# Kernel optimization log

Hardware: AMD Instinct MI355X
Metric: run time of the kernel (lower is better)

Reference implementation:

```python
import jax, jax.numpy as jnp
import numpy as np

EPS = 1e-16


def setup_inputs() -> dict:
    key = jax.random.key(0)
    k1, k2 = jax.random.split(key)
    p = jax.random.normal(k1, (2, 32, 2048, 4), dtype=jnp.float32)
    q = jax.random.normal(k2, (32, 2048, 4), dtype=jnp.float32)
    return {"p": p, "q": q}


def reference(p, q):
    # im=False path: take the real part of the complex generated momenta
    p_real = p[0]                      # (B, N, 4)
    # loss_norm_choice='p3', take_sqrt=True: use 3-momenta (drop energy)
    p3 = p_real[..., 1:]               # (B, N, 3)
    q3 = q[..., 1:]                    # (B, M, 3)
    # Pairwise Euclidean distance (cdist) via the expanded quadratic form to
    # avoid materializing the (B, N, M, 3) difference tensor.
    x2 = jnp.sum(p3 * p3, axis=-1)     # (B, N)
    y2 = jnp.sum(q3 * q3, axis=-1)     # (B, M)
    xy = jnp.einsum('bnd,bmd->bnm', p3, q3)  # (B, N, M)
    dist_sq = x2[..., :, None] + y2[..., None, :] - 2.0 * xy
    dist = jnp.sqrt(jnp.maximum(dist_sq, 0.0) + EPS)  # (B, N, M)
    # Bidirectional nearest-neighbor min-reduction
    min_pq = jnp.min(dist, axis=-1)    # (B, N)
    min_qp = jnp.min(dist, axis=-2)    # (B, M)
    chamfer_loss = jnp.sum((min_pq + min_qp) * 0.5)
    return chamfer_loss
```

## Files before the change

kernel.cpp:

```cpp
#include <hip/hip_runtime.h>
#include <math.h>


#define NPTS   2048
#define NBATCH 32
#define NTOT   (2 * NBATCH * NPTS)
#define EPSF   1e-16f
#define BIGF   3.4e38f

__device__ __forceinline__ float min3f(float a, float b, float c) {
    return fminf(fminf(a, b), c);
}

__global__ __launch_bounds__(256) void chamfer_tile_kernel(
    const float* __restrict__ P, const float* __restrict__ Q,
    unsigned int* __restrict__ ws)
{
    __shared__ float4 sp[256];
    __shared__ float4 sq[256];
    __shared__ float  scol[4][256];

    const int tid = threadIdx.x;
    const int tx  = tid & 15;
    const int ty  = tid >> 4;
    const int bi  = blockIdx.x;
    const int bj  = blockIdx.y;
    const int b   = blockIdx.z;

    {
        float4 pv = ((const float4*)P)[(size_t)b * NPTS + bi * 256 + tid];
        sp[tid] = make_float4(pv.y, pv.z, pv.w,
                              pv.y*pv.y + pv.z*pv.z + pv.w*pv.w);
        float4 qv = ((const float4*)Q)[(size_t)b * NPTS + bj * 256 + tid];
        sq[tid] = make_float4(-2.f*qv.y, -2.f*qv.z, -2.f*qv.w,
                              qv.y*qv.y + qv.z*qv.z + qv.w*qv.w);
    }
    __syncthreads();

    float px[16], py[16], pz[16], x2[16];
    #pragma unroll
    for (int k = 0; k < 16; ++k) {
        float4 v = sp[ty + 16 * k];
        px[k] = v.x; py[k] = v.y; pz[k] = v.z; x2[k] = v.w;
    }

    float rowacc[16], colacc[16];
    #pragma unroll
    for (int k = 0; k < 16; ++k) { rowacc[k] = BIGF; colacc[k] = BIGF; }

    for (int jp = 0; jp < 8; ++jp) {
        float4 q0 = sq[tx + 32 * jp];
        float4 q1 = sq[tx + 32 * jp + 16];
        float c0 = BIGF, c1 = BIGF;
        #pragma unroll
        for (int k = 0; k < 16; k += 2) {
            float t00 = fmaf(px[k],   q0.x, fmaf(py[k],   q0.y, pz[k]   * q0.z));
            float t01 = fmaf(px[k],   q1.x, fmaf(py[k],   q1.y, pz[k]   * q1.z));
            float t10 = fmaf(px[k+1], q0.x, fmaf(py[k+1], q0.y, pz[k+1] * q0.z));
            float t11 = fmaf(px[k+1], q1.x, fmaf(py[k+1], q1.y, pz[k+1] * q1.z));
            rowacc[k]   = min3f(rowacc[k],   t00 + q0.w, t01 + q1.w);
            rowacc[k+1] = min3f(rowacc[k+1], t10 + q0.w, t11 + q1.w);
            c0 = min3f(c0, t00 + x2[k], t10 + x2[k+1]);
            c1 = min3f(c1, t01 + x2[k], t11 + x2[k+1]);
        }
        colacc[2*jp]     = c0;
        colacc[2*jp + 1] = c1;
    }

    #pragma unroll
    for (int k = 0; k < 16; ++k) {
        float v = rowacc[k];
        v = fminf(v, __shfl_xor(v, 1));
        v = fminf(v, __shfl_xor(v, 2));
        v = fminf(v, __shfl_xor(v, 4));
        v = fminf(v, __shfl_xor(v, 8));
        rowacc[k] = v;
    }
    if (tx == 0) {
        #pragma unroll
        for (int k = 0; k < 16; ++k) {
            float d2 = fmaxf(x2[k] + rowacc[k], 0.f);
            atomicMin(&ws[b * NPTS + bi * 256 + (ty + 16 * k)],
                      __float_as_uint(d2));
        }
    }

    #pragma unroll
    for (int j = 0; j < 16; ++j) {
        float v = colacc[j];
        v = fminf(v, __shfl_xor(v, 16));
        v = fminf(v, __shfl_xor(v, 32));
        colacc[j] = v;
    }
    {
        const int wv   = tid >> 6;
        const int lane = tid & 63;
        if (lane < 16) {
            #pragma unroll
            for (int j = 0; j < 16; ++j) scol[wv][j * 16 + lane] = colacc[j];
        }
    }
    __syncthreads();
    {
        const int c = tid;
        float v = fminf(fminf(scol[0][c], scol[1][c]),
                        fminf(scol[2][c], scol[3][c]));
        float d2 = fmaxf(v + sq[c].w, 0.f);
        atomicMin(&ws[NBATCH * NPTS + b * NPTS + bj * 256 + c],
                  __float_as_uint(d2));
    }
}

__global__ __launch_bounds__(256) void chamfer_sum_kernel(
    const unsigned int* __restrict__ ws, float* __restrict__ out)
{
    __shared__ float rbuf[4];
    const int tid = threadIdx.x;
    const int i0  = blockIdx.x * 256 + tid;

    float s = 0.f;
    for (int i = i0; i < NTOT; i += gridDim.x * 256)
        s += sqrtf(__uint_as_float(ws[i]) + EPSF);

    #pragma unroll
    for (int off = 32; off > 0; off >>= 1) s += __shfl_down(s, off);
    if ((tid & 63) == 0) rbuf[tid >> 6] = s;
    __syncthreads();
    if (tid == 0)
        atomicAdd(out, 0.5f * ((rbuf[0] + rbuf[1]) + (rbuf[2] + rbuf[3])));
}

extern "C" void kernel_launch(void* const* d_in, const int* in_sizes, int n_in,
                              void* d_out, int out_size, void* d_ws, size_t ws_size,
                              hipStream_t stream) {
    const float* P = (const float*)d_in[0];
    const float* Q = (const float*)d_in[1];
    float* out = (float*)d_out;
    unsigned int* ws = (unsigned int*)d_ws;

    hipMemsetAsync(ws, 0x7F, (size_t)NTOT * sizeof(unsigned int), stream);
    hipMemsetAsync(out, 0, sizeof(float), stream);

    dim3 grid(NPTS / 256, NPTS / 256, NBATCH);
    chamfer_tile_kernel<<<grid, 256, 0, stream>>>(P, Q, ws);

    chamfer_sum_kernel<<<128, 256, 0, stream>>>(ws, out);
}
```

Before: 84.22 us.

## Compute pairwise squared distances with split-bf16 MFMA instead of scalar FMAs

Recasts the pairwise distance computation as a matrix product on the matrix cores. Each point's coordinates and squared norm are split into high and low bf16 parts packed along the K dimension. A 16x16x32 bf16 MFMA then yields x2+y2-2xy directly for each tile, and row and column minima are reduced from the accumulator registers. This removes most scalar FMA work, at the cost of split-bf16 precision error, K-lanes wasted on zero padding, and extra packing work.

```diff
diff --git a/kernel.cpp b/kernel.cpp
--- a/kernel.cpp
+++ b/kernel.cpp
@@ -8,105 +8,141 @@
 #define EPSF   1e-16f
 #define BIGF   3.4e38f
 
-__device__ __forceinline__ float min3f(float a, float b, float c) {
-    return fminf(fminf(a, b), c);
+typedef short bf16x8 __attribute__((ext_vector_type(8)));
+typedef float f32x4  __attribute__((ext_vector_type(4)));
+
+__device__ __forceinline__ short f2b(float f) {
+    unsigned u = __float_as_uint(f);
+    return (short)((u + 0x7FFFu + ((u >> 16) & 1u)) >> 16);
+}
+__device__ __forceinline__ float b2f(short h) {
+    return __uint_as_float(((unsigned)(unsigned short)h) << 16);
 }
 
-__global__ __launch_bounds__(256) void chamfer_tile_kernel(
+__global__ __launch_bounds__(256) void chamfer_mfma_kernel(
     const float* __restrict__ P, const float* __restrict__ Q,
     unsigned int* __restrict__ ws)
 {
-    __shared__ float4 sp[256];
-    __shared__ float4 sq[256];
-    __shared__ float  scol[4][256];
+    __shared__ short sA[256 * 16];
+    __shared__ short sB[256 * 16];
+    __shared__ float scol[4][256];
 
-    const int tid = threadIdx.x;
-    const int tx  = tid & 15;
-    const int ty  = tid >> 4;
-    const int bi  = blockIdx.x;
-    const int bj  = blockIdx.y;
-    const int b   = blockIdx.z;
+    const int tid  = threadIdx.x;
+    const int w    = tid >> 6;
+    const int lane = tid & 63;
+    const int l15  = lane & 15;
+    const int kc   = lane >> 4;
+    const int bi   = blockIdx.x;
+    const int bj   = blockIdx.y;
+    const int b    = blockIdx.z;
 
     {
         float4 pv = ((const float4*)P)[(size_t)b * NPTS + bi * 256 + tid];
-        sp[tid] = make_float4(pv.y, pv.z, pv.w,
-                              pv.y*pv.y + pv.z*pv.z + pv.w*pv.w);
         float4 qv = ((const float4*)Q)[(size_t)b * NPTS + bj * 256 + tid];
-        sq[tid] = make_float4(-2.f*qv.y, -2.f*qv.z, -2.f*qv.w,
-                              qv.y*qv.y + qv.z*qv.z + qv.w*qv.w);
+        const short one = f2b(1.0f);
+
+        float px = pv.y, py = pv.z, pz = pv.w;
+        float x2 = px*px + py*py + pz*pz;
+        short x2h = f2b(x2),  x2l = f2b(x2 - b2f(x2h));
+        short phx = f2b(px),  plx = f2b(px - b2f(phx));
+        short phy = f2b(py),  ply = f2b(py - b2f(phy));
+        short phz = f2b(pz),  plz = f2b(pz - b2f(phz));
+        short mhx = f2b(-2.f * b2f(phx)), mlx = f2b(-2.f * b2f(plx));
+        short mhy = f2b(-2.f * b2f(phy)), mly = f2b(-2.f * b2f(ply));
+        short mhz = f2b(-2.f * b2f(phz)), mlz = f2b(-2.f * b2f(plz));
+        __align__(16) short a[16] = { x2h, x2l, one, one,
+                                      mhx, mhy, mhz, mhx, mhy, mhz,
+                                      mlx, mly, mlz, mlx, mly, mlz };
+
+        float qx = qv.y, qy = qv.z, qz = qv.w;
+        float y2 = qx*qx + qy*qy + qz*qz;
+        short y2h = f2b(y2),  y2l = f2b(y2 - b2f(y2h));
+        short qhx = f2b(qx),  qlx = f2b(qx - b2f(qhx));
+        short qhy = f2b(qy),  qly = f2b(qy - b2f(qhy));
+        short qhz = f2b(qz),  qlz = f2b(qz - b2f(qhz));
+        __align__(16) short bb[16] = { one, one, y2h, y2l,
+                                       qhx, qhy, qhz, qlx, qly, qlz,
+                                       qhx, qhy, qhz, qlx, qly, qlz };
+
+        *(uint4*)&sA[tid * 16]     = *(const uint4*)&a[0];
+        *(uint4*)&sA[tid * 16 + 8] = *(const uint4*)&a[8];
+        *(uint4*)&sB[tid * 16]     = *(const uint4*)&bb[0];
+        *(uint4*)&sB[tid * 16 + 8] = *(const uint4*)&bb[8];
     }
     __syncthreads();
 
-    float px[16], py[16], pz[16], x2[16];
+    const bf16x8 zf = {0, 0, 0, 0, 0, 0, 0, 0};
+    bf16x8 Af[4];
     #pragma unroll
-    for (int k = 0; k < 16; ++k) {
-        float4 v = sp[ty + 16 * k];
-        px[k] = v.x; py[k] = v.y; pz[k] = v.z; x2[k] = v.w;
+    for (int r = 0; r < 4; ++r) {
+        const int pt = w * 64 + r * 16 + l15;
+        Af[r] = (kc < 2) ? *(const bf16x8*)&sA[pt * 16 + kc * 8] : zf;
     }
 
-    float rowacc[16], colacc[16];
+    float rowmin[4][4], colmin[16];
     #pragma unroll
-    for (int k = 0; k < 16; ++k) { rowacc[k] = BIGF; colacc[k] = BIGF; }
-
-    for (int jp = 0; jp < 8; ++jp) {
-        float4 q0 = sq[tx + 32 * jp];
-        float4 q1 = sq[tx + 32 * jp + 16];
-        float c0 = BIGF, c1 = BIGF;
+    for (int r = 0; r < 4; ++r)
         #pragma unroll
-        for (int k = 0; k < 16; k += 2) {
-            float t00 = fmaf(px[k],   q0.x, fmaf(py[k],   q0.y, pz[k]   * q0.z));
-            float t01 = fmaf(px[k],   q1.x, fmaf(py[k],   q1.y, pz[k]   * q1.z));
-            float t10 = fmaf(px[k+1], q0.x, fmaf(py[k+1], q0.y, pz[k+1] * q0.z));
-            float t11 = fmaf(px[k+1], q1.x, fmaf(py[k+1], q1.y, pz[k+1] * q1.z));
-            rowacc[k]   = min3f(rowacc[k],   t00 + q0.w, t01 + q1.w);
-            rowacc[k+1] = min3f(rowacc[k+1], t10 + q0.w, t11 + q1.w);
-            c0 = min3f(c0, t00 + x2[k], t10 + x2[k+1]);
-            c1 = min3f(c1, t01 + x2[k], t11 + x2[k+1]);
-        }
-        colacc[2*jp]     = c0;
-        colacc[2*jp + 1] = c1;
-    }
+        for (int g = 0; g < 4; ++g) rowmin[r][g] = BIGF;
+    #pragma unroll
+    for (int j = 0; j < 16; ++j) colmin[j] = BIGF;
 
     #pragma unroll
-    for (int k = 0; k < 16; ++k) {
-        float v = rowacc[k];
-        v = fminf(v, __shfl_xor(v, 1));
-        v = fminf(v, __shfl_xor(v, 2));
-        v = fminf(v, __shfl_xor(v, 4));
-        v = fminf(v, __shfl_xor(v, 8));
-        rowacc[k] = v;
-    }
-    if (tx == 0) {
+    for (int j = 0; j < 16; ++j) {
+        const int pt = j * 16 + l15;
+        bf16x8 Bf = (kc < 2) ? *(const bf16x8*)&sB[pt * 16 + kc * 8] : zf;
         #pragma unroll
-        for (int k = 0; k < 16; ++k) {
-            float d2 = fmaxf(x2[k] + rowacc[k], 0.f);
-            atomicMin(&ws[b * NPTS + bi * 256 + (ty + 16 * k)],
-                      __float_as_uint(d2));
+        for (int r = 0; r < 4; ++r) {
+            f32x4 c = {0.f, 0.f, 0.f, 0.f};
+            c = __builtin_amdgcn_mfma_f32_16x16x32_bf16(Af[r], Bf, c, 0, 0, 0);
+            rowmin[r][0] = fminf(rowmin[r][0], c[0]);
+            rowmin[r][1] = fminf(rowmin[r][1], c[1]);
+            rowmin[r][2] = fminf(rowmin[r][2], c[2]);
+            rowmin[r][3] = fminf(rowmin[r][3], c[3]);
+            colmin[j] = fminf(colmin[j],
+                              fminf(fminf(c[0], c[1]), fminf(c[2], c[3])));
         }
     }
 
     #pragma unroll
+    for (int r = 0; r < 4; ++r)
+        #pragma unroll
+        for (int g = 0; g < 4; ++g) {
+            float v = rowmin[r][g];
+            v = fminf(v, __shfl_xor(v, 1));
+            v = fminf(v, __shfl_xor(v, 2));
+            v = fminf(v, __shfl_xor(v, 4));
+            v = fminf(v, __shfl_xor(v, 8));
+            rowmin[r][g] = v;
+        }
+    if (l15 == 0) {
+        #pragma unroll
+        for (int r = 0; r < 4; ++r)
+            #pragma unroll
+            for (int g = 0; g < 4; ++g) {
+                const int row = bi * 256 + w * 64 + r * 16 + (lane >> 4) * 4 + g;
+                float d2 = fmaxf(rowmin[r][g], 0.f);
+                atomicMin(&ws[b * NPTS + row], __float_as_uint(d2));
+            }
+    }
+
+    #pragma unroll
     for (int j = 0; j < 16; ++j) {
-        float v = colacc[j];
+        float v = colmin[j];
         v = fminf(v, __shfl_xor(v, 16));
         v = fminf(v, __shfl_xor(v, 32));
-        colacc[j] = v;
+        colmin[j] = v;
     }
-    {
-        const int wv   = tid >> 6;
-        const int lane = tid & 63;
-        if (lane < 16) {
-            #pragma unroll
-            for (int j = 0; j < 16; ++j) scol[wv][j * 16 + lane] = colacc[j];
-        }
+    if (lane < 16) {
+        #pragma unroll
+        for (int j = 0; j < 16; ++j) scol[w][j * 16 + lane] = colmin[j];
     }
     __syncthreads();
     {
-        const int c = tid;
-        float v = fminf(fminf(scol[0][c], scol[1][c]),
-                        fminf(scol[2][c], scol[3][c]));
-        float d2 = fmaxf(v + sq[c].w, 0.f);
-        atomicMin(&ws[NBATCH * NPTS + b * NPTS + bj * 256 + c],
+        float v = fminf(fminf(scol[0][tid], scol[1][tid]),
+                        fminf(scol[2][tid], scol[3][tid]));
+        float d2 = fmaxf(v, 0.f);
+        atomicMin(&ws[NBATCH * NPTS + b * NPTS + bj * 256 + tid],
                   __float_as_uint(d2));
     }
 }
@@ -142,7 +178,7 @@
     hipMemsetAsync(out, 0, sizeof(float), stream);
 
     dim3 grid(NPTS / 256, NPTS / 256, NBATCH);
-    chamfer_tile_kernel<<<grid, 256, 0, stream>>>(P, Q, ws);
+    chamfer_mfma_kernel<<<grid, 256, 0, stream>>>(P, Q, ws);
 
     chamfer_sum_kernel<<<128, 256, 0, stream>>>(ws, out);
 }
```

Measured after the change: 111.4 us. 32.2% more time.
